# Performance work log

Hardware: AMD Instinct MI355X
Metric: run time of the kernel (lower is better)

Reference implementation:

```python
import math
import jax, jax.numpy as jnp
import numpy as np

T, N, D = 8, 1024, 128  # num_timestamps, tot_nodes, node_input_size

def setup_inputs() -> dict:
    key = jax.random.key(0)
    k1, k2 = jax.random.split(key)
    raw_features = jax.random.normal(k1, (T, N, D), dtype=jnp.float32)
    adj = jax.random.randint(k2, (N, N), 0, 2, dtype=jnp.int32)
    return {"raw_features": raw_features, "adj": adj}

def reference(raw_features, adj):
    t, n, d = raw_features.shape
    scale = 1.0 / math.sqrt(d)
    # --- GAT: adjacency-masked self-attention per timestamp ---
    scores = jnp.einsum('tnd,tmd->tnm', raw_features, raw_features) * scale  # [T,N,N]
    masked = jnp.where(adj[None] > 0, scores, jnp.float32(-1e12))
    attention = jax.nn.softmax(masked, axis=2)
    node_features = jnp.einsum('tnm,tmd->tnd', attention, raw_features)      # [T,N,D]
    # --- temporal scores per node ---
    spatial_features = node_features.transpose(1, 0, 2)                      # [N,T,D]
    temp_scores = jnp.einsum('ntd,nsd->nts', spatial_features, spatial_features) * scale
    spatial_weights = jax.nn.sigmoid(temp_scores)                            # [N,T,T]
    # --- repeat(N,1,1).view(N,N,T,T) == broadcast over leading axis: ST[i,j] = sw[j] ---
    ST = jnp.broadcast_to(spatial_weights[None], (n, n, t, t))               # [N,N,T,T]
    ST = ST.transpose(3, 1, 2, 0)                                            # [T,N,T,N]
    return ST.reshape(t * n, t * n)
```

## Files before the change

### kernel.cpp

```cpp
#include <hip/hip_runtime.h>
#include <hip/hip_bf16.h>
#include <math.h>

#define T 8
#define N 1024
#define D 128

constexpr float SCALE = 0.08838834764831845f;

typedef __attribute__((ext_vector_type(8))) short short8;
typedef __attribute__((ext_vector_type(4))) float floatx4;

#define MFMA16(a, b, c) __builtin_amdgcn_mfma_f32_16x16x32_bf16((a), (b), (c), 0, 0, 0)

__global__ __launch_bounds__(256) void convert_bf16(const float* __restrict__ X,
                                                    ushort* __restrict__ XB,
                                                    ushort* __restrict__ XBT_hi,
                                                    ushort* __restrict__ XBT_lo) {
    const int t  = blockIdx.y;
    const int n0 = blockIdx.x * 64;
    const int tid = threadIdx.x;

    __shared__ ushort Hi[128][66];
    __shared__ ushort Lo[128][66];

    #pragma unroll
    for (int r = 0; r < 8; ++r) {
        int idx = r * 256 + tid;
        int nl  = idx >> 5;
        int c4  = idx & 31;
        float4 v = *(const float4*)(X + ((size_t)t * N + n0 + nl) * D + c4 * 4);
        float vv[4] = {v.x, v.y, v.z, v.w};
        ushort4 o; ushort* op = (ushort*)&o;
        #pragma unroll
        for (int k = 0; k < 4; ++k) {
            __hip_bfloat16 h = __float2bfloat16(vv[k]);
            float hf = __bfloat162float(h);
            __hip_bfloat16 l = __float2bfloat16(vv[k] - hf);
            op[k] = *(ushort*)&h;
            Hi[c4 * 4 + k][nl] = *(ushort*)&h;
            Lo[c4 * 4 + k][nl] = *(ushort*)&l;
        }
        *(ushort4*)(XB + ((size_t)t * N + n0 + nl) * D + c4 * 4) = o;
    }
    __syncthreads();

    const int u  = tid & 31;
    const int dr = tid >> 5;
    #pragma unroll
    for (int p = 0; p < 16; ++p) {
        int d = p * 8 + dr;
        uint hv = *(const uint*)&Hi[d][2 * u];
        uint lv = *(const uint*)&Lo[d][2 * u];
        int n_lo = 2 * u;
        int g8   = (n0 + n_lo) >> 3;
        int pos  = n_lo & 7;
        size_t off = (((size_t)t * 128 + g8) * 128 + d) * 8 + pos;
        *(uint*)(XBT_hi + off) = hv;
        *(uint*)(XBT_lo + off) = lv;
    }
}

__global__ __launch_bounds__(256) void pack_adj(const int* __restrict__ adj,
                                                ushort* __restrict__ Abits) {
    int g = blockIdx.x * 256 + threadIdx.x;
    int i = g >> 6, w = g & 63;
    const int4* p4 = (const int4*)(adj + (size_t)i * N + w * 16);
    uint m16 = 0;
    #pragma unroll
    for (int v4 = 0; v4 < 4; ++v4) {
        int4 v = p4[v4];
        m16 |= (v.x != 0 ? 1u : 0u) << (v4 * 4 + 0);
        m16 |= (v.y != 0 ? 1u : 0u) << (v4 * 4 + 1);
        m16 |= (v.z != 0 ? 1u : 0u) << (v4 * 4 + 2);
        m16 |= (v.w != 0 ? 1u : 0u) << (v4 * 4 + 3);
    }
    Abits[g] = (ushort)m16;
}

__global__ __launch_bounds__(512, 4) void attn_fused(const ushort* __restrict__ XB,
                                                     const ushort* __restrict__ XBT_hi,
                                                     const ushort* __restrict__ XBT_lo,
                                                     const ushort* __restrict__ Abits,
                                                     float* __restrict__ NF) {
    const int g  = blockIdx.x;
    const int t  = g & 7;
    const int i0 = (g >> 3) * 16;
    const int tid  = threadIdx.x;
    const int wid  = tid >> 6;
    const int lane = tid & 63;
    const int m    = lane & 15;
    const int quad = lane >> 4;
    const int jbase = wid * 128;

    __shared__ ushort Ph[16][1024];
    __shared__ ushort Plo[16][1024];
    float* red = (float*)&Ph[0][0];

    const ushort* Xt = XB + (size_t)t * N * D;

    short8 afrag[4];
    {
        const ushort* pa = Xt + (size_t)(i0 + m) * D + quad * 8;
        #pragma unroll
        for (int kq = 0; kq < 4; ++kq) afrag[kq] = *(const short8*)(pa + kq * 32);
    }

    floatx4 acc[8];
    #pragma unroll
    for (int c = 0; c < 8; ++c) acc[c] = (floatx4){0.f, 0.f, 0.f, 0.f};

    short8 bfr[2][4];
    {
        const ushort* pb = Xt + (size_t)(jbase + m) * D + quad * 8;
        bfr[0][0] = *(const short8*)(pb);
        bfr[0][1] = *(const short8*)(pb + 32);
        bfr[0][2] = *(const short8*)(pb + 64);
        bfr[0][3] = *(const short8*)(pb + 96);
    }
    #pragma unroll
    for (int c = 0; c < 8; ++c) {
        if (c < 7) {
            const ushort* pb = Xt + (size_t)(jbase + 16 * (c + 1) + m) * D + quad * 8;
            bfr[(c + 1) & 1][0] = *(const short8*)(pb);
            bfr[(c + 1) & 1][1] = *(const short8*)(pb + 32);
            bfr[(c + 1) & 1][2] = *(const short8*)(pb + 64);
            bfr[(c + 1) & 1][3] = *(const short8*)(pb + 96);
        }
        acc[c] = MFMA16(afrag[0], bfr[c & 1][0], acc[c]);
        acc[c] = MFMA16(afrag[1], bfr[c & 1][1], acc[c]);
        acc[c] = MFMA16(afrag[2], bfr[c & 1][2], acc[c]);
        acc[c] = MFMA16(afrag[3], bfr[c & 1][3], acc[c]);
    }

    short8 adjw[4];
    #pragma unroll
    for (int q = 0; q < 4; ++q)
        adjw[q] = *(const short8*)(Abits + (size_t)(i0 + quad * 4 + q) * 64 + wid * 8);
    #pragma unroll
    for (int q = 0; q < 4; ++q) {
        #pragma unroll
        for (int c = 0; c < 8; ++c) {
            int aw = (ushort)adjw[q][c];
            acc[c][q] = ((aw >> m) & 1) ? acc[c][q] * SCALE : -1e12f;
        }
    }

    float mx[4], inv[4];
    #pragma unroll
    for (int q = 0; q < 4; ++q) {
        float v_ = acc[0][q];
        #pragma unroll
        for (int c = 1; c < 8; ++c) v_ = fmaxf(v_, acc[c][q]);
        v_ = fmaxf(v_, __shfl_xor(v_, 1));
        v_ = fmaxf(v_, __shfl_xor(v_, 2));
        v_ = fmaxf(v_, __shfl_xor(v_, 4));
        v_ = fmaxf(v_, __shfl_xor(v_, 8));
        mx[q] = v_;
    }
    if (m == 0) {
        #pragma unroll
        for (int q = 0; q < 4; ++q) red[wid * 16 + quad * 4 + q] = mx[q];
    }
    __syncthreads();
    #pragma unroll
    for (int q = 0; q < 4; ++q) {
        int r = quad * 4 + q;
        float v_ = red[r];
        #pragma unroll
        for (int w = 1; w < 8; ++w) v_ = fmaxf(v_, red[w * 16 + r]);
        mx[q] = v_;
    }

    float sm[4];
    #pragma unroll
    for (int q = 0; q < 4; ++q) {
        float s_ = 0.f;
        #pragma unroll
        for (int c = 0; c < 8; ++c) {
            float p = __expf(acc[c][q] - mx[q]);
            acc[c][q] = p;
            s_ += p;
        }
        s_ += __shfl_xor(s_, 1);
        s_ += __shfl_xor(s_, 2);
        s_ += __shfl_xor(s_, 4);
        s_ += __shfl_xor(s_, 8);
        sm[q] = s_;
    }
    if (m == 0) {
        #pragma unroll
        for (int q = 0; q < 4; ++q) red[128 + wid * 16 + quad * 4 + q] = sm[q];
    }
    __syncthreads();
    #pragma unroll
    for (int q = 0; q < 4; ++q) {
        int r = quad * 4 + q;
        float s_ = red[128 + r];
        #pragma unroll
        for (int w = 1; w < 8; ++w) s_ += red[128 + w * 16 + r];
        inv[q] = 1.f / s_;
    }
    __syncthreads();

    #pragma unroll
    for (int q = 0; q < 4; ++q) {
        const int row = quad * 4 + q;
        #pragma unroll
        for (int c = 0; c < 8; ++c) {
            const int col = jbase + 16 * c + m;
            const int sc = ((((col >> 3) ^ (row & 7)) << 3) | (col & 7));
            float p = acc[c][q] * inv[q];
            __hip_bfloat16 h = __float2bfloat16(p);
            float hf = __bfloat162float(h);
            __hip_bfloat16 l = __float2bfloat16(p - hf);
            Ph[row][sc]  = *(ushort*)&h;
            Plo[row][sc] = *(ushort*)&l;
        }
    }
    __syncthreads();

    const int dcol = wid * 16 + m;
    const ushort* ph_base = XBT_hi + (size_t)t * 131072 + (size_t)dcol * 8;
    const ushort* pl_base = XBT_lo + (size_t)t * 131072 + (size_t)dcol * 8;
    short8 pfh[4], pfl[4];
#define PF(kq_)                                                                  \
    {                                                                            \
        const size_t off_ = (size_t)((kq_) * 4 + quad) * 1024;                   \
        pfh[(kq_) & 3] = *(const short8*)(ph_base + off_);                       \
        pfl[(kq_) & 3] = *(const short8*)(pl_base + off_);                       \
    }
    PF(0); PF(1); PF(2);

    floatx4 accN = (floatx4){0.f, 0.f, 0.f, 0.f};
    #pragma unroll
    for (int kq = 0; kq < 32; ++kq) {
        if (kq < 29) PF(kq + 3);
        const int blk = (((kq * 4 + quad) ^ (m & 7)) << 3);
        short8 ah = *(const short8*)&Ph[m][blk];
        short8 al = *(const short8*)&Plo[m][blk];
        accN = MFMA16(ah, pfh[kq & 3], accN);
        accN = MFMA16(ah, pfl[kq & 3], accN);
        accN = MFMA16(al, pfh[kq & 3], accN);
    }
#undef PF

    float* NFt = NF + (size_t)t * N * D;
    #pragma unroll
    for (int q = 0; q < 4; ++q)
        NFt[(size_t)(i0 + quad * 4 + q) * D + dcol] = accN[q];
}

__global__ __launch_bounds__(256) void expand_fused(const float* __restrict__ NF,
                                                    float* __restrict__ out) {
    const int row = blockIdx.x;
    const int b = row >> 10, j = row & 1023;
    const int tid = threadIdx.x;

    __shared__ float F[T][D + 4];
    __shared__ float w[T];

    {
        int a = tid >> 5, c4 = (tid & 31) * 4;
        *(float4*)(&F[a][c4]) = *(const float4*)(NF + ((size_t)a * N + j) * D + c4);
    }
    __syncthreads();

    if (tid < T) {
        float s = 0.f;
        #pragma unroll
        for (int d4 = 0; d4 < 32; ++d4) {
            float4 fa = *(const float4*)(&F[tid][d4 * 4]);
            float4 fb = *(const float4*)(&F[b][d4 * 4]);
            s += fa.x * fb.x + fa.y * fb.y + fa.z * fb.z + fa.w * fb.w;
        }
        w[tid] = 1.f / (1.f + __expf(-s * SCALE));
    }
    __syncthreads();

    floatx4* orow = (floatx4*)(out + (size_t)row * (T * N));
    #pragma unroll
    for (int a = 0; a < T; ++a) {
        float wv = w[a];
        floatx4 v = {wv, wv, wv, wv};
        __builtin_nontemporal_store(v, orow + a * 256 + tid);
    }
}

extern "C" void kernel_launch(void* const* d_in, const int* in_sizes, int n_in,
                              void* d_out, int out_size, void* d_ws, size_t ws_size,
                              hipStream_t stream) {
    const float* X   = (const float*)d_in[0];
    const int*   adj = (const int*)d_in[1];
    float* out = (float*)d_out;

    float*  NF     = (float*)d_ws;
    ushort* XB     = (ushort*)(NF + (size_t)T * N * D);
    ushort* XBT_hi = XB + (size_t)T * N * D;
    ushort* XBT_lo = XBT_hi + (size_t)T * N * D;
    ushort* Abits  = XBT_lo + (size_t)T * N * D;

    convert_bf16<<<dim3(N / 64, T), 256, 0, stream>>>(X, XB, XBT_hi, XBT_lo);
    pack_adj<<<dim3(N * 64 / 256), 256, 0, stream>>>(adj, Abits);
    attn_fused<<<dim3((N / 16) * T), 512, 0, stream>>>(XB, XBT_hi, XBT_lo, Abits, NF);
    expand_fused<<<dim3(T * N), 256, 0, stream>>>(NF, out);
}
```

Baseline: 308.1 us.

## Halve attention P buffers in LDS with two-phase staging and raise occupancy

The P matrix staging in shared memory shrinks from 16x1024 to 16x512 hi/lo buffers. The PV product now runs in two halves: waves 0-3 write their half of P, everyone consumes it, then waves 4-7 overwrite the buffer with the second half. This cuts LDS from 64KB to 32KB per block, and launch bounds rise to 6 blocks per CU. The B-fragment double-buffering and the hoisted adjacency loads are dropped to lower register pressure. The cost is two extra barriers and less load/compute overlap in the QK loop.

```diff
diff --git a/kernel.cpp b/kernel.cpp
--- a/kernel.cpp
+++ b/kernel.cpp
@@ -78,7 +78,7 @@
     Abits[g] = (ushort)m16;
 }
 
-__global__ __launch_bounds__(512, 4) void attn_fused(const ushort* __restrict__ XB,
+__global__ __launch_bounds__(512, 6) void attn_fused(const ushort* __restrict__ XB,
                                                      const ushort* __restrict__ XBT_hi,
                                                      const ushort* __restrict__ XBT_lo,
                                                      const ushort* __restrict__ Abits,
@@ -93,8 +93,8 @@
     const int quad = lane >> 4;
     const int jbase = wid * 128;
 
-    __shared__ ushort Ph[16][1024];
-    __shared__ ushort Plo[16][1024];
+    __shared__ ushort Ph[16][512];
+    __shared__ ushort Plo[16][512];
     float* red = (float*)&Ph[0][0];
 
     const ushort* Xt = XB + (size_t)t * N * D;
@@ -110,38 +110,25 @@
     #pragma unroll
     for (int c = 0; c < 8; ++c) acc[c] = (floatx4){0.f, 0.f, 0.f, 0.f};
 
-    short8 bfr[2][4];
-    {
-        const ushort* pb = Xt + (size_t)(jbase + m) * D + quad * 8;
-        bfr[0][0] = *(const short8*)(pb);
-        bfr[0][1] = *(const short8*)(pb + 32);
-        bfr[0][2] = *(const short8*)(pb + 64);
-        bfr[0][3] = *(const short8*)(pb + 96);
-    }
     #pragma unroll
     for (int c = 0; c < 8; ++c) {
-        if (c < 7) {
-            const ushort* pb = Xt + (size_t)(jbase + 16 * (c + 1) + m) * D + quad * 8;
-            bfr[(c + 1) & 1][0] = *(const short8*)(pb);
-            bfr[(c + 1) & 1][1] = *(const short8*)(pb + 32);
-            bfr[(c + 1) & 1][2] = *(const short8*)(pb + 64);
-            bfr[(c + 1) & 1][3] = *(const short8*)(pb + 96);
-        }
-        acc[c] = MFMA16(afrag[0], bfr[c & 1][0], acc[c]);
-        acc[c] = MFMA16(afrag[1], bfr[c & 1][1], acc[c]);
-        acc[c] = MFMA16(afrag[2], bfr[c & 1][2], acc[c]);
-        acc[c] = MFMA16(afrag[3], bfr[c & 1][3], acc[c]);
-    }
-
-    short8 adjw[4];
-    #pragma unroll
-    for (int q = 0; q < 4; ++q)
-        adjw[q] = *(const short8*)(Abits + (size_t)(i0 + quad * 4 + q) * 64 + wid * 8);
-    #pragma unroll
-    for (int q = 0; q < 4; ++q) {
+        const ushort* pb = Xt + (size_t)(jbase + 16 * c + m) * D + quad * 8;
+        short8 b0 = *(const short8*)(pb);
+        short8 b1 = *(const short8*)(pb + 32);
+        short8 b2 = *(const short8*)(pb + 64);
+        short8 b3 = *(const short8*)(pb + 96);
+        acc[c] = MFMA16(afrag[0], b0, acc[c]);
+        acc[c] = MFMA16(afrag[1], b1, acc[c]);
+        acc[c] = MFMA16(afrag[2], b2, acc[c]);
+        acc[c] = MFMA16(afrag[3], b3, acc[c]);
+    }
+
+    #pragma unroll
+    for (int q = 0; q < 4; ++q) {
+        short8 adjw = *(const short8*)(Abits + (size_t)(i0 + quad * 4 + q) * 64 + wid * 8);
         #pragma unroll
         for (int c = 0; c < 8; ++c) {
-            int aw = (ushort)adjw[q][c];
+            int aw = (ushort)adjw[c];
             acc[c][q] = ((aw >> m) & 1) ? acc[c][q] * SCALE : -1e12f;
         }
     }
@@ -200,23 +187,6 @@
         #pragma unroll
         for (int w = 1; w < 8; ++w) s_ += red[128 + w * 16 + r];
         inv[q] = 1.f / s_;
-    }
-    __syncthreads();
-
-    #pragma unroll
-    for (int q = 0; q < 4; ++q) {
-        const int row = quad * 4 + q;
-        #pragma unroll
-        for (int c = 0; c < 8; ++c) {
-            const int col = jbase + 16 * c + m;
-            const int sc = ((((col >> 3) ^ (row & 7)) << 3) | (col & 7));
-            float p = acc[c][q] * inv[q];
-            __hip_bfloat16 h = __float2bfloat16(p);
-            float hf = __bfloat162float(h);
-            __hip_bfloat16 l = __float2bfloat16(p - hf);
-            Ph[row][sc]  = *(ushort*)&h;
-            Plo[row][sc] = *(ushort*)&l;
-        }
     }
     __syncthreads();
 
@@ -232,10 +202,29 @@
     }
     PF(0); PF(1); PF(2);
 
+    if (wid < 4) {
+        #pragma unroll
+        for (int q = 0; q < 4; ++q) {
+            const int row = quad * 4 + q;
+            #pragma unroll
+            for (int c = 0; c < 8; ++c) {
+                const int col = jbase + 16 * c + m;
+                const int sc = ((((col >> 3) ^ (row & 7)) << 3) | (col & 7));
+                float p = acc[c][q] * inv[q];
+                __hip_bfloat16 h = __float2bfloat16(p);
+                float hf = __bfloat162float(h);
+                __hip_bfloat16 l = __float2bfloat16(p - hf);
+                Ph[row][sc]  = *(ushort*)&h;
+                Plo[row][sc] = *(ushort*)&l;
+            }
+        }
+    }
+    __syncthreads();
+
     floatx4 accN = (floatx4){0.f, 0.f, 0.f, 0.f};
     #pragma unroll
-    for (int kq = 0; kq < 32; ++kq) {
-        if (kq < 29) PF(kq + 3);
+    for (int kq = 0; kq < 16; ++kq) {
+        PF(kq + 3);
         const int blk = (((kq * 4 + quad) ^ (m & 7)) << 3);
         short8 ah = *(const short8*)&Ph[m][blk];
         short8 al = *(const short8*)&Plo[m][blk];
@@ -243,6 +232,37 @@
         accN = MFMA16(ah, pfl[kq & 3], accN);
         accN = MFMA16(al, pfh[kq & 3], accN);
     }
+    __syncthreads();
+
+    if (wid >= 4) {
+        #pragma unroll
+        for (int q = 0; q < 4; ++q) {
+            const int row = quad * 4 + q;
+            #pragma unroll
+            for (int c = 0; c < 8; ++c) {
+                const int col = (jbase + 16 * c + m) & 511;
+                const int sc = ((((col >> 3) ^ (row & 7)) << 3) | (col & 7));
+                float p = acc[c][q] * inv[q];
+                __hip_bfloat16 h = __float2bfloat16(p);
+                float hf = __bfloat162float(h);
+                __hip_bfloat16 l = __float2bfloat16(p - hf);
+                Ph[row][sc]  = *(ushort*)&h;
+                Plo[row][sc] = *(ushort*)&l;
+            }
+        }
+    }
+    __syncthreads();
+
+    #pragma unroll
+    for (int kq = 16; kq < 32; ++kq) {
+        if (kq < 29) PF(kq + 3);
+        const int blk = ((((kq - 16) * 4 + quad) ^ (m & 7)) << 3);
+        short8 ah = *(const short8*)&Ph[m][blk];
+        short8 al = *(const short8*)&Plo[m][blk];
+        accN = MFMA16(ah, pfh[kq & 3], accN);
+        accN = MFMA16(ah, pfl[kq & 3], accN);
+        accN = MFMA16(al, pfh[kq & 3], accN);
+    }
 #undef PF
 
     float* NFt = NF + (size_t)t * N * D;
```

After: 345.0 us. 12.0% more time.
